# Kernel optimization log

Measured on AMD Instinct MI355X. Metric: run time of the kernel, lower is better.

Reference implementation:

```python
import math
import jax, jax.numpy as jnp
import numpy as np

NUM_BUCKETS = 32
MAX_DISTANCE = 128


def _relative_position_bucket(relative_position, num_buckets=NUM_BUCKETS,
                              bidirectional=True, max_distance=MAX_DISTANCE):
    """T5 relative-position bucketing (Mesh-TF), int32 in/out."""
    relative_buckets = jnp.zeros_like(relative_position)
    if bidirectional:
        num_buckets //= 2
        relative_buckets = (relative_position > 0).astype(jnp.int32) * num_buckets
        relative_position = jnp.abs(relative_position)
    else:
        relative_position = -jnp.minimum(relative_position, 0)
    max_exact = num_buckets // 2
    is_small = relative_position < max_exact
    # clamp to >=1 to avoid log(0); those entries are selected by the small branch
    rp_f = jnp.maximum(relative_position, 1).astype(jnp.float32)
    rel_if_large = max_exact + (
        jnp.log(rp_f / max_exact) / math.log(max_distance / max_exact)
        * (num_buckets - max_exact)
    ).astype(jnp.int32)
    rel_if_large = jnp.minimum(rel_if_large, num_buckets - 1)
    return relative_buckets + jnp.where(is_small, relative_position, rel_if_large)


def _compute_bias(bias_table, qlen, klen, bidirectional=True):
    context_position = jnp.arange(qlen, dtype=jnp.int32)[:, None]
    memory_position = jnp.arange(klen, dtype=jnp.int32)[None, :]
    relative_position = memory_position - context_position          # [Q, K]
    rp_bucket = _relative_position_bucket(relative_position, bidirectional=bidirectional)
    values = bias_table[rp_bucket]                                   # [Q, K, H]
    return jnp.transpose(values, (2, 0, 1))[None]                    # [1, H, Q, K]


def setup_inputs() -> dict:
    key = jax.random.key(0)
    k1, k2, k3, k4, k5 = jax.random.split(key, 5)
    B, H, S, D = 2, 8, 2048, 64
    return {
        "query": jax.random.normal(k1, (B, H, S, D), dtype=jnp.float32),
        "key": jax.random.normal(k2, (B, H, S, D), dtype=jnp.float32),
        "value": jax.random.normal(k3, (B, H, S, D), dtype=jnp.float32),
        "mask": jax.random.randint(k4, (B, 1, 1, S), 0, 2, dtype=jnp.int32),
        "bias_table": jax.random.normal(k5, (NUM_BUCKETS, H), dtype=jnp.float32),
    }


def reference(query, key, value, mask, bias_table):
    qlen, klen = query.shape[-2], key.shape[-2]
    dk = jnp.asarray(key.shape[-1], dtype=jnp.float32)
    logits = jnp.einsum("bhqd,bhkd->bhqk", query, key) / jnp.sqrt(dk)
    logits = logits + _compute_bias(bias_table, qlen, klen, bidirectional=True)
    logits = logits + mask.astype(jnp.float32) * -1e9
    attention_weights = jax.nn.softmax(logits, axis=-1)              # [B,H,Q,K]
    output = jnp.einsum("bhqk,bhkd->bhqd", attention_weights, value)
    return output, attention_weights
```

## Files before the change

### kernel.cpp

```cpp
#include <hip/hip_runtime.h>
#include <math.h>

constexpr int Bc = 2, Hc = 8, Sc = 2048, Dc = 64;
constexpr int BQ = 64;
constexpr int KT = 64;
constexpr int NKT = Sc / KT;

using bf16x8  = __attribute__((ext_vector_type(8))) short;
using f32x4   = __attribute__((ext_vector_type(4))) float;
using short4v = __attribute__((ext_vector_type(4))) short;

__device__ __forceinline__ short f2b(float f) {
  union { float f; unsigned u; } v; v.f = f;
  unsigned u = v.u;
  return (short)((u + 0x7FFFu + ((u >> 16) & 1u)) >> 16);
}

__device__ __forceinline__ int swzs(int row, int colShorts) {
  int byte = (colShorts << 1) ^ ((row & 7) << 4);
  return (row << 6) + (byte >> 1);
}

__device__ __forceinline__ int bucket_of(int rp) {
  int bck = (rp > 0) ? 16 : 0;
  int a = rp < 0 ? -rp : rp;
  int lb;
  if      (a <  8) lb = a;
  else if (a < 12) lb = 8;
  else if (a < 16) lb = 9;
  else if (a < 23) lb = 10;
  else if (a < 32) lb = 11;
  else if (a < 46) lb = 12;
  else if (a < 64) lb = 13;
  else if (a < 91) lb = 14;
  else             lb = 15;
  return bck + lb;
}

__global__ __launch_bounds__(512, 4)
void t5_attn_kernel(const float* __restrict__ Q, const float* __restrict__ K,
                    const float* __restrict__ V, const int* __restrict__ mask,
                    const float* __restrict__ bias_table,
                    float* __restrict__ out0,
                    float* __restrict__ out1)
{
  __shared__ short Ktl[64 * 64];
  __shared__ short Vtl[64 * 64];
  __shared__ short Ptl[64 * 64];
  __shared__ float biasl[128];
  __shared__ float maskl[64];
  __shared__ float stats[8][16][2];

  const int tid  = threadIdx.x;
  const int lane = tid & 63;
  const int wid  = tid >> 6;
  const int bh   = blockIdx.x >> 5;
  const int qt   = blockIdx.x & 31;
  const int b    = bh >> 3, h = bh & 7;
  const int q0   = qt * BQ;

  const float* Qb = Q + (size_t)bh * Sc * Dc;
  const float* Kb = K + (size_t)bh * Sc * Dc;
  const float* Vb = V + (size_t)bh * Sc * Dc;

  const int mt  = wid >> 1;
  const int ntA = (wid & 1) * 2;
  const int l16 = lane & 15, lh = lane >> 4;

  bf16x8 aq0, aq1;
  {
    const float* qrow = Qb + (size_t)(q0 + mt * 16 + l16) * Dc + lh * 8;
    #pragma unroll
    for (int i = 0; i < 8; ++i) { aq0[i] = f2b(qrow[i]); aq1[i] = f2b(qrow[i + 32]); }
  }

  auto stage_k = [&](int k0) {
    #pragma unroll
    for (int r = 0; r < 2; ++r) {
      int idx = tid + r * 512;
      int krow = idx >> 4, dq = (idx & 15) << 2;
      float4 v = *reinterpret_cast<const float4*>(Kb + (size_t)(k0 + krow) * Dc + dq);
      short4v sv; sv[0] = f2b(v.x); sv[1] = f2b(v.y); sv[2] = f2b(v.z); sv[3] = f2b(v.w);
      *reinterpret_cast<short4v*>(&Ktl[swzs(krow, dq)]) = sv;
    }
  };
  auto stage_v = [&](int k0) {
    int krow0 = wid << 3;
    #pragma unroll
    for (int r = 0; r < 8; r += 4) {
      short4v sv;
      #pragma unroll
      for (int rr = 0; rr < 4; ++rr)
        sv[rr] = f2b(Vb[(size_t)(k0 + krow0 + r + rr) * Dc + lane]);
      *reinterpret_cast<short4v*>(&Vtl[swzs(lane, krow0 + r)]) = sv;
    }
  };
  auto stage_bm = [&](int k0) {
    if (tid < 128)      biasl[tid] = bias_table[bucket_of(k0 - q0 + tid - 63) * Hc + h];
    else if (tid < 192) maskl[tid - 128] = -1e9f * (float)mask[b * Sc + k0 + (tid - 128)];
  };

  auto qk_tile = [&](int nt, float lout[4]) {
    bf16x8 b0 = *reinterpret_cast<const bf16x8*>(&Ktl[swzs(nt * 16 + l16, lh * 8)]);
    bf16x8 b1 = *reinterpret_cast<const bf16x8*>(&Ktl[swzs(nt * 16 + l16, 32 + lh * 8)]);
    f32x4 acc = {0.f, 0.f, 0.f, 0.f};
    acc = __builtin_amdgcn_mfma_f32_16x16x32_bf16(aq0, b0, acc, 0, 0, 0);
    acc = __builtin_amdgcn_mfma_f32_16x16x32_bf16(aq1, b1, acc, 0, 0, 0);
    int lc = nt * 16 + l16;
    float mval = maskl[lc];
    #pragma unroll
    for (int j = 0; j < 4; ++j) {
      int rl = mt * 16 + lh * 4 + j;
      lout[j] = acc[j] * 0.125f + biasl[lc - rl + 63] + mval;
    }
  };

  float mL[4], sL[4];
  #pragma unroll
  for (int j = 0; j < 4; ++j) { mL[j] = -__builtin_inff(); sL[j] = 0.f; }

  for (int kt = 0; kt < NKT; ++kt) {
    int k0 = kt * KT;
    __syncthreads();
    stage_k(k0); stage_bm(k0);
    __syncthreads();
    float l0[4], l1[4];
    qk_tile(ntA,     l0);
    qk_tile(ntA + 1, l1);
    #pragma unroll
    for (int j = 0; j < 4; ++j) {
      float a  = fmaxf(l0[j], l1[j]);
      float mn = fmaxf(mL[j], a);
      sL[j] = sL[j] * __expf(mL[j] - mn) + __expf(l0[j] - mn) + __expf(l1[j] - mn);
      mL[j] = mn;
    }
  }

  float mx[4], sm[4];
  #pragma unroll
  for (int j = 0; j < 4; ++j) {
    float m = mL[j], s = sL[j];
    #pragma unroll
    for (int off = 1; off < 16; off <<= 1) {
      float mo = __shfl_xor(m, off, 64);
      float so = __shfl_xor(s, off, 64);
      float M  = fmaxf(m, mo);
      s = s * __expf(m - M) + so * __expf(mo - M);
      m = M;
    }
    mx[j] = m; sm[j] = s;
  }

  __syncthreads();
  if (l16 == 0) {
    #pragma unroll
    for (int j = 0; j < 4; ++j) { stats[wid][lh * 4 + j][0] = mx[j]; stats[wid][lh * 4 + j][1] = sm[j]; }
  }
  __syncthreads();
  float Mf[4], Zi[4];
  {
    int pw = wid ^ 1;
    #pragma unroll
    for (int j = 0; j < 4; ++j) {
      float m2 = stats[pw][lh * 4 + j][0], s2 = stats[pw][lh * 4 + j][1];
      float M = fmaxf(mx[j], m2);
      float Z = sm[j] * __expf(mx[j] - M) + s2 * __expf(m2 - M);
      Mf[j] = M; Zi[j] = 1.0f / Z;
    }
  }

  f32x4 oa0 = {0.f, 0.f, 0.f, 0.f}, oa1 = {0.f, 0.f, 0.f, 0.f};
  float* W = out1 + (size_t)bh * Sc * Sc;

  for (int kt = 0; kt < NKT; ++kt) {
    int k0 = kt * KT;
    __syncthreads();
    stage_k(k0); stage_v(k0); stage_bm(k0);
    __syncthreads();
    #pragma unroll
    for (int t = 0; t < 2; ++t) {
      int nt = ntA + t;
      float lv[4];
      qk_tile(nt, lv);
      int lc = nt * 16 + l16;
      #pragma unroll
      for (int j = 0; j < 4; ++j) {
        int rl = mt * 16 + lh * 4 + j;
        float p = __expf(lv[j] - Mf[j]) * Zi[j];
        W[(size_t)(q0 + rl) * Sc + k0 + lc] = p;
        Ptl[swzs(rl, lc)] = f2b(p);
      }
    }
    __syncthreads();
    {
      bf16x8 pa0 = *reinterpret_cast<const bf16x8*>(&Ptl[swzs(mt * 16 + l16, lh * 8)]);
      bf16x8 pa1 = *reinterpret_cast<const bf16x8*>(&Ptl[swzs(mt * 16 + l16, 32 + lh * 8)]);
      #pragma unroll
      for (int t = 0; t < 2; ++t) {
        int no = ntA + t;
        bf16x8 vb0 = *reinterpret_cast<const bf16x8*>(&Vtl[swzs(no * 16 + l16, lh * 8)]);
        bf16x8 vb1 = *reinterpret_cast<const bf16x8*>(&Vtl[swzs(no * 16 + l16, 32 + lh * 8)]);
        f32x4& oa = t ? oa1 : oa0;
        oa = __builtin_amdgcn_mfma_f32_16x16x32_bf16(pa0, vb0, oa, 0, 0, 0);
        oa = __builtin_amdgcn_mfma_f32_16x16x32_bf16(pa1, vb1, oa, 0, 0, 0);
      }
    }
  }

  float* O = out0 + (size_t)bh * Sc * Dc;
  #pragma unroll
  for (int t = 0; t < 2; ++t) {
    f32x4 oa = t ? oa1 : oa0;
    int col = (ntA + t) * 16 + l16;
    #pragma unroll
    for (int j = 0; j < 4; ++j) {
      int row = q0 + mt * 16 + lh * 4 + j;
      O[(size_t)row * Dc + col] = oa[j];
    }
  }
}

extern "C" void kernel_launch(void* const* d_in, const int* in_sizes, int n_in,
                              void* d_out, int out_size, void* d_ws, size_t ws_size,
                              hipStream_t stream) {
  const float* Q  = (const float*)d_in[0];
  const float* K  = (const float*)d_in[1];
  const float* V  = (const float*)d_in[2];
  const int*   mk = (const int*)d_in[3];
  const float* bt = (const float*)d_in[4];
  float* out0 = (float*)d_out;
  float* out1 = out0 + (size_t)Bc * Hc * Sc * Dc;

  dim3 grid(16 * 32), block(512);
  hipLaunchKernelGGL(t5_attn_kernel, grid, block, 0, stream, Q, K, V, mk, bt, out0, out1);
}
```

Measured before the change: 429.2 us.

## Restructure attention kernel with 4 waves, double-buffered K/V and vectorized weight stores

Moves to 256-thread blocks where each wave owns 16 query rows and all 64 key columns, which removes the cross-wave softmax stats exchange. K and V tiles are double-buffered in LDS with register prefetch of the next tile, so there is one barrier per iteration instead of two. Mask and bias for the whole key range are precomputed once per block, and the block index is remapped. The attention-weight output is now written as bf16-rounded values reread from LDS, using 16-byte nontemporal stores, which trades fp32 precision in the weights for coalesced writes.

New measurement: 390.2 us. -9.1%, faster.

```diff
diff --git a/kernel.cpp b/kernel.cpp
--- a/kernel.cpp
+++ b/kernel.cpp
@@ -1,4 +1,5 @@
 #include <hip/hip_runtime.h>
+#include <hip/hip_bf16.h>
 #include <math.h>
 
 constexpr int Bc = 2, Hc = 8, Sc = 2048, Dc = 64;
@@ -6,21 +7,30 @@
 constexpr int KT = 64;
 constexpr int NKT = Sc / KT;
 
-using bf16x8  = __attribute__((ext_vector_type(8))) short;
-using f32x4   = __attribute__((ext_vector_type(4))) float;
-using short4v = __attribute__((ext_vector_type(4))) short;
+using bf16x8 = __attribute__((ext_vector_type(8))) short;
+using f32x4  = __attribute__((ext_vector_type(4))) float;
+using uint2v = __attribute__((ext_vector_type(2))) unsigned;
 
 __device__ __forceinline__ short f2b(float f) {
   union { float f; unsigned u; } v; v.f = f;
   unsigned u = v.u;
   return (short)((u + 0x7FFFu + ((u >> 16) & 1u)) >> 16);
 }
-
+__device__ __forceinline__ unsigned pk2(float a, float b) {
+  union { __hip_bfloat162 h; unsigned u; } v;
+  v.h = __float22bfloat162_rn(make_float2(a, b));
+  return v.u;
+}
+__device__ __forceinline__ float b2f_lo(unsigned u) {
+  union { unsigned u; float f; } v; v.u = u << 16; return v.f;
+}
+__device__ __forceinline__ float b2f_hi(unsigned u) {
+  union { unsigned u; float f; } v; v.u = u & 0xFFFF0000u; return v.f;
+}
 __device__ __forceinline__ int swzs(int row, int colShorts) {
   int byte = (colShorts << 1) ^ ((row & 7) << 4);
   return (row << 6) + (byte >> 1);
 }
-
 __device__ __forceinline__ int bucket_of(int rp) {
   int bck = (rp > 0) ? 16 : 0;
   int a = rp < 0 ? -rp : rp;
@@ -37,25 +47,24 @@
   return bck + lb;
 }
 
-__global__ __launch_bounds__(512, 4)
+__global__ __launch_bounds__(256, 3)
 void t5_attn_kernel(const float* __restrict__ Q, const float* __restrict__ K,
                     const float* __restrict__ V, const int* __restrict__ mask,
                     const float* __restrict__ bias_table,
                     float* __restrict__ out0,
                     float* __restrict__ out1)
 {
-  __shared__ short Ktl[64 * 64];
-  __shared__ short Vtl[64 * 64];
-  __shared__ short Ptl[64 * 64];
-  __shared__ float biasl[128];
-  __shared__ float maskl[64];
-  __shared__ float stats[8][16][2];
+  __shared__ __align__(16) short Kbuf[2][64 * 64];
+  __shared__ __align__(16) short Vbuf[2][64 * 64];
+  __shared__ __align__(16) short Ptl[64 * 64];
+  __shared__ short maskAll[Sc];
+  __shared__ float biasD[BQ + Sc - 1];
 
   const int tid  = threadIdx.x;
   const int lane = tid & 63;
   const int wid  = tid >> 6;
-  const int bh   = blockIdx.x >> 5;
-  const int qt   = blockIdx.x & 31;
+  const int sbid = (blockIdx.x & 7) * 64 + (blockIdx.x >> 3);
+  const int bh   = sbid >> 5, qt = sbid & 31;
   const int b    = bh >> 3, h = bh & 7;
   const int q0   = qt * BQ;
 
@@ -63,80 +72,103 @@
   const float* Kb = K + (size_t)bh * Sc * Dc;
   const float* Vb = V + (size_t)bh * Sc * Dc;
 
-  const int mt  = wid >> 1;
-  const int ntA = (wid & 1) * 2;
   const int l16 = lane & 15, lh = lane >> 4;
 
+  auto ld_k = [&](int k0, float4 r[4]) {
+    #pragma unroll
+    for (int rr = 0; rr < 4; ++rr) {
+      int unit = rr * 256 + tid;
+      int row = unit >> 4, c4 = unit & 15;
+      r[rr] = *reinterpret_cast<const float4*>(Kb + (size_t)(k0 + row) * Dc + c4 * 4);
+    }
+  };
+  auto st_k = [&](short* buf, float4 r[4]) {
+    #pragma unroll
+    for (int rr = 0; rr < 4; ++rr) {
+      int unit = rr * 256 + tid;
+      int row = unit >> 4, c4 = unit & 15;
+      uint2v w; w[0] = pk2(r[rr].x, r[rr].y); w[1] = pk2(r[rr].z, r[rr].w);
+      *reinterpret_cast<uint2v*>(&buf[swzs(row, c4 * 4)]) = w;
+    }
+  };
+  auto ld_v = [&](int k0, float vr[16]) {
+    int kb0 = k0 + wid * 16;
+    #pragma unroll
+    for (int rr = 0; rr < 16; ++rr)
+      vr[rr] = Vb[(size_t)(kb0 + rr) * Dc + lane];
+  };
+  auto st_v = [&](short* buf, float vr[16]) {
+    #pragma unroll
+    for (int r = 0; r < 16; r += 4) {
+      uint2v w; w[0] = pk2(vr[r], vr[r + 1]); w[1] = pk2(vr[r + 2], vr[r + 3]);
+      *reinterpret_cast<uint2v*>(&buf[swzs(lane, wid * 16 + r)]) = w;
+    }
+  };
+
+  float4 kst[4];
+  ld_k(0, kst);
+  {
+    const int4* mrow = reinterpret_cast<const int4*>(mask + (size_t)b * Sc);
+    #pragma unroll
+    for (int r = 0; r < 2; ++r) {
+      int4 m = mrow[r * 256 + tid];
+      int base = (r * 256 + tid) * 4;
+      maskAll[base + 0] = (short)m.x; maskAll[base + 1] = (short)m.y;
+      maskAll[base + 2] = (short)m.z; maskAll[base + 3] = (short)m.w;
+    }
+    for (int i = tid; i < BQ + Sc - 1; i += 256)
+      biasD[i] = bias_table[bucket_of(i - q0 - 63) * Hc + h];
+  }
   bf16x8 aq0, aq1;
   {
-    const float* qrow = Qb + (size_t)(q0 + mt * 16 + l16) * Dc + lh * 8;
+    const float* qrow = Qb + (size_t)(q0 + wid * 16 + l16) * Dc + lh * 8;
     #pragma unroll
     for (int i = 0; i < 8; ++i) { aq0[i] = f2b(qrow[i]); aq1[i] = f2b(qrow[i + 32]); }
   }
-
-  auto stage_k = [&](int k0) {
-    #pragma unroll
-    for (int r = 0; r < 2; ++r) {
-      int idx = tid + r * 512;
-      int krow = idx >> 4, dq = (idx & 15) << 2;
-      float4 v = *reinterpret_cast<const float4*>(Kb + (size_t)(k0 + krow) * Dc + dq);
-      short4v sv; sv[0] = f2b(v.x); sv[1] = f2b(v.y); sv[2] = f2b(v.z); sv[3] = f2b(v.w);
-      *reinterpret_cast<short4v*>(&Ktl[swzs(krow, dq)]) = sv;
-    }
-  };
-  auto stage_v = [&](int k0) {
-    int krow0 = wid << 3;
-    #pragma unroll
-    for (int r = 0; r < 8; r += 4) {
-      short4v sv;
+  st_k(Kbuf[0], kst);
+  __syncthreads();
+
+  const int rlb = wid * 16 + lh * 4;
+
+  float mL[4], sL[4];
+  #pragma unroll
+  for (int j = 0; j < 4; ++j) { mL[j] = -__builtin_inff(); sL[j] = 0.f; }
+
+  for (int t = 0; t < NKT; ++t) {
+    int k0 = t * KT;
+    ld_k(((t + 1) & (NKT - 1)) * KT, kst);
+    const short* kb = Kbuf[t & 1];
+    float l[4][4];
+    #pragma unroll
+    for (int nt = 0; nt < 4; ++nt) {
+      bf16x8 b0 = *reinterpret_cast<const bf16x8*>(&kb[swzs(nt * 16 + l16, lh * 8)]);
+      bf16x8 b1 = *reinterpret_cast<const bf16x8*>(&kb[swzs(nt * 16 + l16, 32 + lh * 8)]);
+      f32x4 acc = {0.f, 0.f, 0.f, 0.f};
+      acc = __builtin_amdgcn_mfma_f32_16x16x32_bf16(aq0, b0, acc, 0, 0, 0);
+      acc = __builtin_amdgcn_mfma_f32_16x16x32_bf16(aq1, b1, acc, 0, 0, 0);
+      int kc = k0 + nt * 16 + l16;
+      float msk = (float)maskAll[kc] * -1e9f;
+      int bbase = kc - rlb + 63;
       #pragma unroll
-      for (int rr = 0; rr < 4; ++rr)
-        sv[rr] = f2b(Vb[(size_t)(k0 + krow0 + r + rr) * Dc + lane]);
-      *reinterpret_cast<short4v*>(&Vtl[swzs(lane, krow0 + r)]) = sv;
-    }
-  };
-  auto stage_bm = [&](int k0) {
-    if (tid < 128)      biasl[tid] = bias_table[bucket_of(k0 - q0 + tid - 63) * Hc + h];
-    else if (tid < 192) maskl[tid - 128] = -1e9f * (float)mask[b * Sc + k0 + (tid - 128)];
-  };
-
-  auto qk_tile = [&](int nt, float lout[4]) {
-    bf16x8 b0 = *reinterpret_cast<const bf16x8*>(&Ktl[swzs(nt * 16 + l16, lh * 8)]);
-    bf16x8 b1 = *reinterpret_cast<const bf16x8*>(&Ktl[swzs(nt * 16 + l16, 32 + lh * 8)]);
-    f32x4 acc = {0.f, 0.f, 0.f, 0.f};
-    acc = __builtin_amdgcn_mfma_f32_16x16x32_bf16(aq0, b0, acc, 0, 0, 0);
-    acc = __builtin_amdgcn_mfma_f32_16x16x32_bf16(aq1, b1, acc, 0, 0, 0);
-    int lc = nt * 16 + l16;
-    float mval = maskl[lc];
+      for (int j = 0; j < 4; ++j)
+        l[nt][j] = acc[j] * 0.125f + biasD[bbase - j] + msk;
+    }
     #pragma unroll
     for (int j = 0; j < 4; ++j) {
-      int rl = mt * 16 + lh * 4 + j;
-      lout[j] = acc[j] * 0.125f + biasl[lc - rl + 63] + mval;
-    }
-  };
-
-  float mL[4], sL[4];
-  #pragma unroll
-  for (int j = 0; j < 4; ++j) { mL[j] = -__builtin_inff(); sL[j] = 0.f; }
-
-  for (int kt = 0; kt < NKT; ++kt) {
-    int k0 = kt * KT;
+      float a01 = fmaxf(l[0][j], l[1][j]), a23 = fmaxf(l[2][j], l[3][j]);
+      float mn  = fmaxf(mL[j], fmaxf(a01, a23));
+      sL[j] = sL[j] * __expf(mL[j] - mn)
+            + __expf(l[0][j] - mn) + __expf(l[1][j] - mn)
+            + __expf(l[2][j] - mn) + __expf(l[3][j] - mn);
+      mL[j] = mn;
+    }
+    st_k(Kbuf[(t + 1) & 1], kst);
     __syncthreads();
-    stage_k(k0); stage_bm(k0);
-    __syncthreads();
-    float l0[4], l1[4];
-    qk_tile(ntA,     l0);
-    qk_tile(ntA + 1, l1);
-    #pragma unroll
-    for (int j = 0; j < 4; ++j) {
-      float a  = fmaxf(l0[j], l1[j]);
-      float mn = fmaxf(mL[j], a);
-      sL[j] = sL[j] * __expf(mL[j] - mn) + __expf(l0[j] - mn) + __expf(l1[j] - mn);
-      mL[j] = mn;
-    }
-  }
-
-  float mx[4], sm[4];
+  }
+
+  float vst[16];
+  ld_v(0, vst);
+  float Mf[4], Zi[4];
   #pragma unroll
   for (int j = 0; j < 4; ++j) {
     float m = mL[j], s = sL[j];
@@ -148,74 +180,76 @@
       s = s * __expf(m - M) + so * __expf(mo - M);
       m = M;
     }
-    mx[j] = m; sm[j] = s;
-  }
-
+    Mf[j] = m; Zi[j] = 1.0f / s;
+  }
+  st_v(Vbuf[0], vst);
   __syncthreads();
-  if (l16 == 0) {
-    #pragma unroll
-    for (int j = 0; j < 4; ++j) { stats[wid][lh * 4 + j][0] = mx[j]; stats[wid][lh * 4 + j][1] = sm[j]; }
-  }
-  __syncthreads();
-  float Mf[4], Zi[4];
-  {
-    int pw = wid ^ 1;
-    #pragma unroll
-    for (int j = 0; j < 4; ++j) {
-      float m2 = stats[pw][lh * 4 + j][0], s2 = stats[pw][lh * 4 + j][1];
-      float M = fmaxf(mx[j], m2);
-      float Z = sm[j] * __expf(mx[j] - M) + s2 * __expf(m2 - M);
-      Mf[j] = M; Zi[j] = 1.0f / Z;
-    }
-  }
-
-  f32x4 oa0 = {0.f, 0.f, 0.f, 0.f}, oa1 = {0.f, 0.f, 0.f, 0.f};
+
+  f32x4 oa[4];
+  #pragma unroll
+  for (int od = 0; od < 4; ++od) oa[od] = f32x4{0.f, 0.f, 0.f, 0.f};
   float* W = out1 + (size_t)bh * Sc * Sc;
 
-  for (int kt = 0; kt < NKT; ++kt) {
-    int k0 = kt * KT;
-    __syncthreads();
-    stage_k(k0); stage_v(k0); stage_bm(k0);
-    __syncthreads();
-    #pragma unroll
-    for (int t = 0; t < 2; ++t) {
-      int nt = ntA + t;
-      float lv[4];
-      qk_tile(nt, lv);
+  for (int t = 0; t < NKT; ++t) {
+    int k0 = t * KT;
+    bool pf = (t + 1 < NKT);
+    if (pf) { ld_k((t + 1) * KT, kst); ld_v((t + 1) * KT, vst); }
+    const short* kb = Kbuf[t & 1];
+    const short* vb = Vbuf[t & 1];
+
+    #pragma unroll
+    for (int nt = 0; nt < 4; ++nt) {
+      bf16x8 b0 = *reinterpret_cast<const bf16x8*>(&kb[swzs(nt * 16 + l16, lh * 8)]);
+      bf16x8 b1 = *reinterpret_cast<const bf16x8*>(&kb[swzs(nt * 16 + l16, 32 + lh * 8)]);
+      f32x4 acc = {0.f, 0.f, 0.f, 0.f};
+      acc = __builtin_amdgcn_mfma_f32_16x16x32_bf16(aq0, b0, acc, 0, 0, 0);
+      acc = __builtin_amdgcn_mfma_f32_16x16x32_bf16(aq1, b1, acc, 0, 0, 0);
+      int kc = k0 + nt * 16 + l16;
+      float msk = (float)maskAll[kc] * -1e9f;
+      int bbase = kc - rlb + 63;
       int lc = nt * 16 + l16;
       #pragma unroll
       for (int j = 0; j < 4; ++j) {
-        int rl = mt * 16 + lh * 4 + j;
-        float p = __expf(lv[j] - Mf[j]) * Zi[j];
-        W[(size_t)(q0 + rl) * Sc + k0 + lc] = p;
-        Ptl[swzs(rl, lc)] = f2b(p);
+        float lv = acc[j] * 0.125f + biasD[bbase - j] + msk;
+        float p  = __expf(lv - Mf[j]) * Zi[j];
+        Ptl[swzs(wid * 16 + lh * 4 + j, lc)] = f2b(p);
       }
     }
+
+    bf16x8 pa0 = *reinterpret_cast<const bf16x8*>(&Ptl[swzs(wid * 16 + l16, lh * 8)]);
+    bf16x8 pa1 = *reinterpret_cast<const bf16x8*>(&Ptl[swzs(wid * 16 + l16, 32 + lh * 8)]);
+    #pragma unroll
+    for (int od = 0; od < 4; ++od) {
+      bf16x8 vb0 = *reinterpret_cast<const bf16x8*>(&vb[swzs(od * 16 + l16, lh * 8)]);
+      bf16x8 vb1 = *reinterpret_cast<const bf16x8*>(&vb[swzs(od * 16 + l16, 32 + lh * 8)]);
+      oa[od] = __builtin_amdgcn_mfma_f32_16x16x32_bf16(pa0, vb0, oa[od], 0, 0, 0);
+      oa[od] = __builtin_amdgcn_mfma_f32_16x16x32_bf16(pa1, vb1, oa[od], 0, 0, 0);
+    }
+
+    #pragma unroll
+    for (int it = 0; it < 4; ++it) {
+      int rloc = it * 4 + lh;
+      uint2v pw = *reinterpret_cast<const uint2v*>(&Ptl[swzs(wid * 16 + rloc, l16 * 4)]);
+      f32x4 wv;
+      wv[0] = b2f_lo(pw[0]); wv[1] = b2f_hi(pw[0]);
+      wv[2] = b2f_lo(pw[1]); wv[3] = b2f_hi(pw[1]);
+      f32x4* dst = reinterpret_cast<f32x4*>(
+          W + (size_t)(q0 + wid * 16 + rloc) * Sc + k0 + l16 * 4);
+      __builtin_nontemporal_store(wv, dst);
+    }
+
+    if (pf) { st_k(Kbuf[(t + 1) & 1], kst); st_v(Vbuf[(t + 1) & 1], vst); }
     __syncthreads();
-    {
-      bf16x8 pa0 = *reinterpret_cast<const bf16x8*>(&Ptl[swzs(mt * 16 + l16, lh * 8)]);
-      bf16x8 pa1 = *reinterpret_cast<const bf16x8*>(&Ptl[swzs(mt * 16 + l16, 32 + lh * 8)]);
-      #pragma unroll
-      for (int t = 0; t < 2; ++t) {
-        int no = ntA + t;
-        bf16x8 vb0 = *reinterpret_cast<const bf16x8*>(&Vtl[swzs(no * 16 + l16, lh * 8)]);
-        bf16x8 vb1 = *reinterpret_cast<const bf16x8*>(&Vtl[swzs(no * 16 + l16, 32 + lh * 8)]);
-        f32x4& oa = t ? oa1 : oa0;
-        oa = __builtin_amdgcn_mfma_f32_16x16x32_bf16(pa0, vb0, oa, 0, 0, 0);
-        oa = __builtin_amdgcn_mfma_f32_16x16x32_bf16(pa1, vb1, oa, 0, 0, 0);
-      }
-    }
   }
 
   float* O = out0 + (size_t)bh * Sc * Dc;
   #pragma unroll
-  for (int t = 0; t < 2; ++t) {
-    f32x4 oa = t ? oa1 : oa0;
-    int col = (ntA + t) * 16 + l16;
+  for (int od = 0; od < 4; ++od) {
+    int col = od * 16 + l16;
     #pragma unroll
     for (int j = 0; j < 4; ++j) {
-      int row = q0 + mt * 16 + lh * 4 + j;
-      O[(size_t)row * Dc + col] = oa[j];
+      int row = q0 + wid * 16 + lh * 4 + j;
+      __builtin_nontemporal_store(oa[od][j], O + (size_t)row * Dc + col);
     }
   }
 }
@@ -231,6 +265,6 @@
   float* out0 = (float*)d_out;
   float* out1 = out0 + (size_t)Bc * Hc * Sc * Dc;
 
-  dim3 grid(16 * 32), block(512);
+  dim3 grid(16 * 32), block(256);
   hipLaunchKernelGGL(t5_attn_kernel, grid, block, 0, stream, Q, K, V, mk, bt, out0, out1);
 }
```
